# Performance work log

Hardware: AMD Instinct MI355X
Metric: run time of the kernel (lower is better)

Reference implementation:

```python
import jax, jax.numpy as jnp
import numpy as np

B, N, X, H = 128, 512, 128, 256  # batch, seq len, in features, hidden

_PARAM_SHAPES = [
    ("fg_w_c", (H,)), ("fg_w_h", (H, H)), ("fg_w_x", (H, X)), ("fg_b", (H,)),
    ("ig_w_c", (H,)), ("ig_w_h", (H, H)), ("ig_w_x", (H, X)), ("ig_b", (H,)),
    ("in_w_h", (H, H)), ("in_w_x", (H, X)), ("in_b", (H,)),
    ("og_w_cn", (H,)), ("og_w_h", (H, H)), ("og_w_x", (H, X)), ("og_b", (H,)), ("og_w_t", (H,)),
    ("tg1_w_x", (H, X)), ("tg1_w_t", (H,)), ("tg1_b", (H,)),
    ("tg2_w_x", (H, X)), ("tg2_w_t", (H,)), ("tg2_b", (H,)),
]


def setup_inputs() -> dict:
    key = jax.random.key(0)
    ks = jax.random.split(key, 2 + len(_PARAM_SHAPES))
    stdv = 1.0 / np.sqrt(H)  # torch __init__ re-inits all params uniform(-stdv, stdv)
    inp = {
        "x": jax.random.normal(ks[0], (B, N, X), jnp.float32),
        "t": jax.random.uniform(ks[1], (B, N, 1), jnp.float32),  # time intervals >= 0
    }
    for i, (name, shape) in enumerate(_PARAM_SHAPES):
        inp[name] = jax.random.uniform(ks[2 + i], shape, jnp.float32, -stdv, stdv)
    return inp


def reference(x, t,
              fg_w_c, fg_w_h, fg_w_x, fg_b,
              ig_w_c, ig_w_h, ig_w_x, ig_b,
              in_w_h, in_w_x, in_b,
              og_w_cn, og_w_h, og_w_x, og_b, og_w_t,
              tg1_w_x, tg1_w_t, tg1_b,
              tg2_w_x, tg2_w_t, tg2_b):
    # TimeLSTM_v3 with nn_type = NN_TYPE_LSTM_TIME2.
    # torch stores vector params as [H,1] and x_cur as [B,xm,1]; here squeezed to [H] / [B,xm].
    # Precompute all input-dependent (non-recurrent) gate terms over the whole sequence: [B,N,H]
    fg_x = jnp.einsum('bnx,hx->bnh', x, fg_w_x) + fg_b
    ig_x = jnp.einsum('bnx,hx->bnh', x, ig_w_x) + ig_b
    in_x = jnp.einsum('bnx,hx->bnh', x, in_w_x) + in_b
    og_x = jnp.einsum('bnx,hx->bnh', x, og_w_x) + og_w_t * t + og_b
    # Time gates depend only on x and t -> fully precomputable
    tm1 = jax.nn.sigmoid(jnp.einsum('bnx,hx->bnh', x, tg1_w_x) + jnp.tanh(tg1_w_t * t) + tg1_b)
    tm2 = jax.nn.sigmoid(jnp.einsum('bnx,hx->bnh', x, tg2_w_x) + jnp.tanh(tg2_w_t * t) + tg2_b)

    def step(carry, inputs):
        h, cm = carry  # each [B,H]
        fg_xt, ig_xt, in_xt, og_xt, tm1_t, tm2_t = inputs
        ig = jax.nn.sigmoid(ig_w_c * cm + h @ ig_w_h.T + ig_xt)
        fg = jax.nn.sigmoid(fg_w_c * cm + h @ fg_w_h.T + fg_xt)
        inn = jnp.tanh(h @ in_w_h.T + in_xt)
        cm_hat = fg * cm + ig * tm1_t * inn
        cm_new = fg * cm + ig * tm2_t * inn
        og = jax.nn.sigmoid(og_w_cn * cm_hat + h @ og_w_h.T + og_xt)
        h_new = og * jnp.tanh(cm_hat)
        return (h_new, cm_new), None

    seqs = tuple(jnp.moveaxis(a, 1, 0) for a in (fg_x, ig_x, in_x, og_x, tm1, tm2))  # [N,B,H]
    init = (jnp.zeros((x.shape[0], H), x.dtype), jnp.zeros((x.shape[0], H), x.dtype))
    (h, cm), _ = jax.lax.scan(step, init, seqs)
    return h, cm  # h: [B,H] (torch squeezes trailing 1), cm: [B,H]
```

## Files before the change

### kernel.cpp

```cpp
#include <hip/hip_runtime.h>
#include <math.h>

#define BATCH 128
#define SEQN  512
#define XF    128
#define HF    256
#define BC    16
#define HC    8
#define TCH   8
#define NBLK  256
#define NTHR  256
#define NGRP  8
#define GSZ   32

#define OFF_WX   0
#define OFF_G    6144
#define OFF_X    12288
#define OFF_CM   28672
#define OFF_TV   28800
#define OFF_COEF 28928
#define OFF_GO   29024
#define LDS_WORDS 29028
#define LDS_BYTES (LDS_WORDS * 4)

struct Params {
  const float* x;
  const float* t;
  const float* w_h[4];
  const float* w_x[6];
  const float* coef[12];
  float* h_buf;
  unsigned* flags;
  unsigned* round;
  float* out;
};

__device__ __forceinline__ float sigmoidf_(float v) { return 1.0f / (1.0f + __expf(-v)); }
__device__ __forceinline__ float tanhf_(float x) {
  const float e = __expf(2.0f * x);
  return 1.0f - 2.0f / (e + 1.0f);
}

__device__ __forceinline__ float swzx1(float v) { return __int_as_float(__builtin_amdgcn_ds_swizzle(__float_as_int(v), 0x041F)); }
__device__ __forceinline__ float swzx2(float v) { return __int_as_float(__builtin_amdgcn_ds_swizzle(__float_as_int(v), 0x081F)); }
__device__ __forceinline__ float swzx4(float v) { return __int_as_float(__builtin_amdgcn_ds_swizzle(__float_as_int(v), 0x101F)); }
__device__ __forceinline__ float swzx8(float v) { return __int_as_float(__builtin_amdgcn_ds_swizzle(__float_as_int(v), 0x201F)); }

__device__ __forceinline__ void post_arrive(unsigned* flags, int gi, int mi, unsigned val) {
  __syncthreads();
  if (threadIdx.x == 0) {
    __hip_atomic_store(&flags[(gi * GSZ + mi) * 16], val,
                       __ATOMIC_RELAXED, __HIP_MEMORY_SCOPE_AGENT);
  }
}

__device__ __forceinline__ void wave_wait(float* sm, const unsigned* flags,
                                          unsigned* round, int gi, int mi,
                                          unsigned target) {
  const int tid = threadIdx.x;
  if (mi == 0) {
    unsigned* go = (unsigned*)&sm[OFF_GO];
    if (tid < 64) {
      const bool need = tid < GSZ;
      const unsigned* f = &flags[(gi * GSZ + (tid & (GSZ - 1))) * 16];
      while (true) {
        unsigned v = need ? __hip_atomic_load(f, __ATOMIC_RELAXED, __HIP_MEMORY_SCOPE_AGENT)
                          : target;
        if (__all((int)(v >= target))) break;
      }
      if (tid == 0) {
        __hip_atomic_store(&round[gi * 16], target,
                           __ATOMIC_RELAXED, __HIP_MEMORY_SCOPE_AGENT);
        __hip_atomic_store(go, target, __ATOMIC_RELAXED, __HIP_MEMORY_SCOPE_WORKGROUP);
      }
    } else {
      while (__hip_atomic_load(go, __ATOMIC_RELAXED, __HIP_MEMORY_SCOPE_WORKGROUP) < target) {}
    }
  } else {
    const unsigned* r = &round[gi * 16];
    while (__hip_atomic_load(r, __ATOMIC_RELAXED, __HIP_MEMORY_SCOPE_AGENT) < target) {}
  }
  asm volatile("" ::: "memory");
}

__global__ __launch_bounds__(NTHR, 1) void timelstm_kernel(Params p) {
  extern __shared__ float sm[];
  const int tid = threadIdx.x;
  const int bid = blockIdx.x;
  const int gi = bid & 7;
  const int mi = bid >> 3;
  const int b0 = gi * BC;
  const int h0 = mi * HC;

  const int lane = tid & 63;
  const int bq = tid >> 6;
  const int kh = lane & 7;
  const int j  = lane >> 3;

  float wrs[4][32];
#pragma unroll
  for (int g = 0; g < 4; ++g)
#pragma unroll
    for (int q = 0; q < 8; ++q) {
      const float4 v = *(const float4*)&p.w_h[g][(size_t)(h0 + j) * HF + kh * 32 + q * 4];
      wrs[g][q * 4 + 0] = v.x; wrs[g][q * 4 + 1] = v.y;
      wrs[g][q * 4 + 2] = v.z; wrs[g][q * 4 + 3] = v.w;
    }
  for (int i = tid; i < 6 * 8 * 128; i += NTHR) {
    int g = i >> 10, jj = (i >> 7) & 7, k = i & 127;
    sm[OFF_WX + k * 48 + jj * 6 + g] = p.w_x[g][(h0 + jj) * XF + k];
  }
  if (tid < 96) sm[OFF_COEF + tid] = p.coef[tid >> 3][h0 + (tid & 7)];
  if (tid < 128) sm[OFF_CM + tid] = 0.0f;
  if (tid == 0) *(unsigned*)&sm[OFF_GO] = 0u;
  if (mi == 0) {
    unsigned long long* hbu = (unsigned long long*)p.h_buf + (size_t)b0 * (HF / 2);
    for (int i = tid; i < BC * HF / 2; i += NTHR) {
      __hip_atomic_store(&hbu[i], 0ull, __ATOMIC_RELAXED, __HIP_MEMORY_SCOPE_AGENT);
    }
  }
  post_arrive(p.flags, gi, mi, 1u);
  unsigned tstep = 1;
  int cur = 0;

  for (int tc0 = 0; tc0 < SEQN; tc0 += TCH) {
    __syncthreads();
    {
#pragma unroll
      for (int half = 0; half < 2; ++half) {
        float4 xr[8];
#pragma unroll
        for (int it = 0; it < 8; ++it) {
          const int ri = (half * 8 + it) * 8 + (tid >> 5);
          xr[it] = *(const float4*)&p.x[((size_t)(b0 + (ri >> 3)) * SEQN + (tc0 + (ri & 7))) * XF + (tid & 31) * 4];
        }
#pragma unroll
        for (int it = 0; it < 8; ++it) {
          const int ri = (half * 8 + it) * 8 + (tid >> 5);
          const int k0 = (tid & 31) * 4;
          const float xb[4] = {xr[it].x, xr[it].y, xr[it].z, xr[it].w};
#pragma unroll
          for (int u = 0; u < 4; ++u) {
            const int k = k0 + u;
            sm[OFF_X + k * 128 + (ri ^ (((k >> 2) & 7) << 2))] = xb[u];
          }
        }
      }
      if (tid < 128)
        sm[OFF_TV + tid] = p.t[(size_t)(b0 + (tid >> 3)) * SEQN + tc0 + (tid & 7)];
    }
    __syncthreads();
    {
      const int c = tid >> 3, r = tid & 7;
      const int c4 = c << 2;
      float a0[4], a1[4], a2[4], a3[4], a4[4], a5[4];
#pragma unroll
      for (int u = 0; u < 4; ++u) { a0[u]=0.f; a1[u]=0.f; a2[u]=0.f; a3[u]=0.f; a4[u]=0.f; a5[u]=0.f; }
      const float* wxp = &sm[OFF_WX + r * 6];
#pragma unroll 4
      for (int k = 0; k < XF; ++k) {
        const float4 xv = *(const float4*)&sm[OFF_X + k * 128 + (c4 ^ (((k >> 2) & 7) << 2))];
        const float2 wA = *(const float2*)&wxp[k * 48 + 0];
        const float2 wB = *(const float2*)&wxp[k * 48 + 2];
        const float2 wC = *(const float2*)&wxp[k * 48 + 4];
        const float xs[4] = {xv.x, xv.y, xv.z, xv.w};
#pragma unroll
        for (int u = 0; u < 4; ++u) {
          a0[u] += wA.x * xs[u]; a1[u] += wA.y * xs[u];
          a2[u] += wB.x * xs[u]; a3[u] += wB.y * xs[u];
          a4[u] += wC.x * xs[u]; a5[u] += wC.y * xs[u];
        }
      }
      const float cfg  = sm[OFF_COEF + 0 * 8 + r], cig  = sm[OFF_COEF + 1 * 8 + r];
      const float cin  = sm[OFF_COEF + 2 * 8 + r];
      const float cogb = sm[OFF_COEF + 3 * 8 + r], cogwt = sm[OFF_COEF + 4 * 8 + r];
      const float ct1w = sm[OFF_COEF + 5 * 8 + r], ct1b = sm[OFF_COEF + 6 * 8 + r];
      const float ct2w = sm[OFF_COEF + 7 * 8 + r], ct2b = sm[OFF_COEF + 8 * 8 + r];
#pragma unroll
      for (int u = 0; u < 4; ++u) {
        const int bt = c4 + u, b = bt >> 3, t = bt & 7;
        const float tv = sm[OFF_TV + bt];
        float* gp = &sm[OFF_G + t * 768 + b * 8 + r];
        gp[0]   = a0[u] + cfg;
        gp[128] = a1[u] + cig;
        gp[256] = a2[u] + cin;
        gp[384] = a3[u] + cogwt * tv + cogb;
        gp[512] = sigmoidf_(a4[u] + tanhf_(ct1w * tv) + ct1b);
        gp[640] = sigmoidf_(a5[u] + tanhf_(ct2w * tv) + ct2b);
      }
    }
    __syncthreads();

    for (int tt = 0; tt < TCH; ++tt) {
      wave_wait(sm, p.flags, p.round, gi, mi, tstep);
      {
        const unsigned long long* hsrc = (const unsigned long long*)
            (p.h_buf + (size_t)cur * BATCH * HF + (size_t)(b0 + (bq << 2)) * HF);
        unsigned long long v[4][2];
#pragma unroll
        for (int u = 0; u < 4; ++u) {
          const unsigned long long* src = hsrc + (size_t)u * (HF / 2) + lane * 2;
          v[u][0] = __hip_atomic_load(src,     __ATOMIC_RELAXED, __HIP_MEMORY_SCOPE_AGENT);
          v[u][1] = __hip_atomic_load(src + 1, __ATOMIC_RELAXED, __HIP_MEMORY_SCOPE_AGENT);
        }
        float f[4][4];
#pragma unroll
        for (int u = 0; u < 4; ++u) {
          union { unsigned long long u64; float2 f2; } x0, x1;
          x0.u64 = v[u][0]; x1.u64 = v[u][1];
          f[u][0] = x0.f2.x; f[u][1] = x0.f2.y; f[u][2] = x1.f2.x; f[u][3] = x1.f2.y;
        }
        const int swz = ((lane >> 3) & 7) << 2;
        const int wbase = OFF_X + (bq << 10);
#pragma unroll
        for (int e = 0; e < 4; ++e) {
          const int a = wbase + (((lane << 4) + (e << 2)) ^ swz);
          float2 lo = {f[0][e], f[1][e]};
          float2 hi = {f[2][e], f[3][e]};
          *(float2*)&sm[a]     = lo;
          *(float2*)&sm[a + 2] = hi;
        }
      }

      float acc[4][4];
#pragma unroll
      for (int bi = 0; bi < 4; ++bi)
#pragma unroll
        for (int g = 0; g < 4; ++g) acc[bi][g] = 0.f;

      const int hbase = OFF_X + (bq << 10) + (kh << 7);
      const int khx = kh << 2;
#pragma unroll
      for (int kk = 0; kk < 32; ++kk) {
        const int off = ((((kk & 7) << 2) ^ khx)) + ((kk >> 3) << 5);
        const float4 hv = *(const float4*)&sm[hbase + off];
        const float w0 = wrs[0][kk], w1 = wrs[1][kk], w2 = wrs[2][kk], w3 = wrs[3][kk];
        acc[0][0] += hv.x * w0; acc[0][1] += hv.x * w1; acc[0][2] += hv.x * w2; acc[0][3] += hv.x * w3;
        acc[1][0] += hv.y * w0; acc[1][1] += hv.y * w1; acc[1][2] += hv.y * w2; acc[1][3] += hv.y * w3;
        acc[2][0] += hv.z * w0; acc[2][1] += hv.z * w1; acc[2][2] += hv.z * w2; acc[2][3] += hv.z * w3;
        acc[3][0] += hv.w * w0; acc[3][1] += hv.w * w1; acc[3][2] += hv.w * w2; acc[3][3] += hv.w * w3;
      }

      const int kb0 = kh & 1, kb1 = (kh >> 1) & 1;
      float s1[2][4];
#pragma unroll
      for (int pp = 0; pp < 2; ++pp)
#pragma unroll
        for (int g = 0; g < 4; ++g) {
          const float mine  = kb0 ? acc[2 * pp + 1][g] : acc[2 * pp][g];
          const float yours = kb0 ? acc[2 * pp][g]     : acc[2 * pp + 1][g];
          s1[pp][g] = mine + swzx1(yours);
        }
      float s2[4];
#pragma unroll
      for (int g = 0; g < 4; ++g) {
        const float mine  = kb1 ? s1[1][g] : s1[0][g];
        const float yours = kb1 ? s1[0][g] : s1[1][g];
        s2[g] = mine + swzx2(yours);
      }
      float pre[4];
#pragma unroll
      for (int g = 0; g < 4; ++g) pre[g] = s2[g] + swzx4(s2[g]);

      {
        const int bi = kh & 3;
        const int b  = (bq << 2) + bi;
        const int ib = b * 8 + j;
        const float cm = sm[OFF_CM + ib];
        const float* gt = &sm[OFF_G + tt * 768 + ib];
        const float fgx = gt[0],   igx = gt[128], inx = gt[256];
        const float ogx = gt[384], tm1 = gt[512], tm2 = gt[640];
        const float igv = sigmoidf_(sm[OFF_COEF + 10 * 8 + j] * cm + pre[1] + igx);
        const float fgv = sigmoidf_(sm[OFF_COEF + 9 * 8 + j] * cm + pre[0] + fgx);
        const float inn = tanhf_(pre[2] + inx);
        const float cbase = fgv * cm, cinn = igv * inn;
        const float cmh = cbase + cinn * tm1;
        const float cmn = cbase + cinn * tm2;
        const float ogv = sigmoidf_(sm[OFF_COEF + 11 * 8 + j] * cmh + pre[3] + ogx);
        const float hn  = ogv * tanhf_(cmh);
        const float hn2 = swzx8(hn);
        if (kh < 4) {
          sm[OFF_CM + ib] = cmn;
          if (!(j & 1)) {
            union { float2 f; unsigned long long u; } cv;
            cv.f.x = hn; cv.f.y = hn2;
            unsigned long long* hdst =
                (unsigned long long*)(p.h_buf + (size_t)(cur ^ 1) * BATCH * HF +
                                      (size_t)(b0 + b) * HF + h0 + j);
            __hip_atomic_store(hdst, cv.u, __ATOMIC_RELAXED, __HIP_MEMORY_SCOPE_AGENT);
          }
          if (tc0 + tt == SEQN - 1) {
            p.out[(size_t)(b0 + b) * HF + h0 + j] = hn;
            p.out[(size_t)BATCH * HF + (size_t)(b0 + b) * HF + h0 + j] = cmn;
          }
        }
      }
      post_arrive(p.flags, gi, mi, tstep + 1);
      ++tstep;
      cur ^= 1;
    }
  }
}

extern "C" void kernel_launch(void* const* d_in, const int* in_sizes, int n_in,
                              void* d_out, int out_size, void* d_ws, size_t ws_size,
                              hipStream_t stream) {
  (void)in_sizes; (void)n_in; (void)out_size; (void)ws_size;
  Params p;
  p.x = (const float*)d_in[0];
  p.t = (const float*)d_in[1];
  p.w_h[0] = (const float*)d_in[3];
  p.w_h[1] = (const float*)d_in[7];
  p.w_h[2] = (const float*)d_in[10];
  p.w_h[3] = (const float*)d_in[14];
  p.w_x[0] = (const float*)d_in[4];
  p.w_x[1] = (const float*)d_in[8];
  p.w_x[2] = (const float*)d_in[11];
  p.w_x[3] = (const float*)d_in[15];
  p.w_x[4] = (const float*)d_in[18];
  p.w_x[5] = (const float*)d_in[21];
  p.coef[0]  = (const float*)d_in[5];
  p.coef[1]  = (const float*)d_in[9];
  p.coef[2]  = (const float*)d_in[12];
  p.coef[3]  = (const float*)d_in[16];
  p.coef[4]  = (const float*)d_in[17];
  p.coef[5]  = (const float*)d_in[19];
  p.coef[6]  = (const float*)d_in[20];
  p.coef[7]  = (const float*)d_in[22];
  p.coef[8]  = (const float*)d_in[23];
  p.coef[9]  = (const float*)d_in[2];
  p.coef[10] = (const float*)d_in[6];
  p.coef[11] = (const float*)d_in[13];
  p.flags = (unsigned*)d_ws;
  p.round = p.flags + NGRP * GSZ * 16;
  p.h_buf = (float*)((char*)d_ws + 32768);
  p.out = (float*)d_out;

  (void)hipMemsetAsync(d_ws, 0, 32768, stream);
  (void)hipFuncSetAttribute((const void*)timelstm_kernel,
                            hipFuncAttributeMaxDynamicSharedMemorySize, LDS_BYTES);
  timelstm_kernel<<<dim3(NBLK), dim3(NTHR), LDS_BYTES, stream>>>(p);
}
```

Baseline: 2.633 ms.

## Replace block-level step barrier with per-wave flag synchronization

Each wave now publishes its own progress flag and waits only on the matching wave (same batch quad) in the other blocks of its group, instead of a __syncthreads plus a single block flag per step. The master block uses one wave per batch quad to poll 32 flags and publishes a per-quad round counter, and the LDS go-word is removed. This is meant to cut the per-timestep cost of a full workgroup barrier and the serialized block-wide handoff on the recurrent critical path. It relies on each wave reading only the h rows its quad wrote, and on s_waitcnt vmcnt(0) with relaxed atomics giving enough ordering, which is a memory-ordering risk.

```diff
diff --git a/kernel.cpp b/kernel.cpp
--- a/kernel.cpp
+++ b/kernel.cpp
@@ -19,8 +19,7 @@
 #define OFF_CM   28672
 #define OFF_TV   28800
 #define OFF_COEF 28928
-#define OFF_GO   29024
-#define LDS_WORDS 29028
+#define LDS_WORDS 29024
 #define LDS_BYTES (LDS_WORDS * 4)
 
 struct Params {
@@ -46,38 +45,28 @@
 __device__ __forceinline__ float swzx4(float v) { return __int_as_float(__builtin_amdgcn_ds_swizzle(__float_as_int(v), 0x101F)); }
 __device__ __forceinline__ float swzx8(float v) { return __int_as_float(__builtin_amdgcn_ds_swizzle(__float_as_int(v), 0x201F)); }
 
-__device__ __forceinline__ void post_arrive(unsigned* flags, int gi, int mi, unsigned val) {
-  __syncthreads();
-  if (threadIdx.x == 0) {
-    __hip_atomic_store(&flags[(gi * GSZ + mi) * 16], val,
+__device__ __forceinline__ void post_wave(unsigned* flags, int gi, int mi, int bq, unsigned val) {
+  asm volatile("s_waitcnt vmcnt(0)" ::: "memory");
+  if ((threadIdx.x & 63) == 0) {
+    __hip_atomic_store(&flags[(gi * GSZ + mi) * 16 + bq], val,
                        __ATOMIC_RELAXED, __HIP_MEMORY_SCOPE_AGENT);
   }
 }
 
-__device__ __forceinline__ void wave_wait(float* sm, const unsigned* flags,
-                                          unsigned* round, int gi, int mi,
+__device__ __forceinline__ void wave_wait(const unsigned* flags, unsigned* round,
+                                          int gi, int mi, int bq, int lane,
                                           unsigned target) {
-  const int tid = threadIdx.x;
   if (mi == 0) {
-    unsigned* go = (unsigned*)&sm[OFF_GO];
-    if (tid < 64) {
-      const bool need = tid < GSZ;
-      const unsigned* f = &flags[(gi * GSZ + (tid & (GSZ - 1))) * 16];
-      while (true) {
-        unsigned v = need ? __hip_atomic_load(f, __ATOMIC_RELAXED, __HIP_MEMORY_SCOPE_AGENT)
-                          : target;
-        if (__all((int)(v >= target))) break;
-      }
-      if (tid == 0) {
-        __hip_atomic_store(&round[gi * 16], target,
-                           __ATOMIC_RELAXED, __HIP_MEMORY_SCOPE_AGENT);
-        __hip_atomic_store(go, target, __ATOMIC_RELAXED, __HIP_MEMORY_SCOPE_WORKGROUP);
-      }
-    } else {
-      while (__hip_atomic_load(go, __ATOMIC_RELAXED, __HIP_MEMORY_SCOPE_WORKGROUP) < target) {}
-    }
+    const unsigned* f = &flags[(gi * GSZ + (lane & 31)) * 16 + bq];
+    while (true) {
+      const unsigned v = __hip_atomic_load(f, __ATOMIC_RELAXED, __HIP_MEMORY_SCOPE_AGENT);
+      if (__all((int)(v >= target))) break;
+    }
+    if (lane == 0)
+      __hip_atomic_store(&round[(gi * 4 + bq) * 16], target,
+                         __ATOMIC_RELAXED, __HIP_MEMORY_SCOPE_AGENT);
   } else {
-    const unsigned* r = &round[gi * 16];
+    const unsigned* r = &round[(gi * 4 + bq) * 16];
     while (__hip_atomic_load(r, __ATOMIC_RELAXED, __HIP_MEMORY_SCOPE_AGENT) < target) {}
   }
   asm volatile("" ::: "memory");
@@ -112,14 +101,17 @@
   }
   if (tid < 96) sm[OFF_COEF + tid] = p.coef[tid >> 3][h0 + (tid & 7)];
   if (tid < 128) sm[OFF_CM + tid] = 0.0f;
-  if (tid == 0) *(unsigned*)&sm[OFF_GO] = 0u;
   if (mi == 0) {
-    unsigned long long* hbu = (unsigned long long*)p.h_buf + (size_t)b0 * (HF / 2);
-    for (int i = tid; i < BC * HF / 2; i += NTHR) {
-      __hip_atomic_store(&hbu[i], 0ull, __ATOMIC_RELAXED, __HIP_MEMORY_SCOPE_AGENT);
-    }
-  }
-  post_arrive(p.flags, gi, mi, 1u);
+    unsigned long long* zb = (unsigned long long*)p.h_buf +
+                             (size_t)(b0 + (bq << 2)) * (HF / 2);
+#pragma unroll
+    for (int q = 0; q < 8; ++q) {
+      __hip_atomic_store(&zb[q * 64 + lane], 0ull,
+                         __ATOMIC_RELAXED, __HIP_MEMORY_SCOPE_AGENT);
+    }
+  }
+  post_wave(p.flags, gi, mi, bq, 1u);
+  __syncthreads();
   unsigned tstep = 1;
   int cur = 0;
 
@@ -192,7 +184,7 @@
     __syncthreads();
 
     for (int tt = 0; tt < TCH; ++tt) {
-      wave_wait(sm, p.flags, p.round, gi, mi, tstep);
+      wave_wait(p.flags, p.round, gi, mi, bq, lane, tstep);
       {
         const unsigned long long* hsrc = (const unsigned long long*)
             (p.h_buf + (size_t)cur * BATCH * HF + (size_t)(b0 + (bq << 2)) * HF);
@@ -295,7 +287,7 @@
           }
         }
       }
-      post_arrive(p.flags, gi, mi, tstep + 1);
+      post_wave(p.flags, gi, mi, bq, tstep + 1);
       ++tstep;
       cur ^= 1;
     }
```

Result: slower. 3.140 ms (+19.2%).

## Prefetch next chunk's x and t into registers during the recurrent steps

Applied to the files above, without the earlier changes.

Global loads of x and t for the next time chunk are issued into registers before the recurrent steps of the current chunk, so their latency overlaps the serial recurrence. The non-recurrent gate projection (phase A) then runs right after the chunk's steps, from registers instead of freshly loaded data. The h staging buffer gets its own LDS region so it no longer aliases the x staging area. The block-wide barriers around phase A are dropped because each wave now writes and reads only its own x rows. This relies on wave-local LDS ordering and adds about 64 more registers per thread.

```diff
diff --git a/kernel.cpp b/kernel.cpp
--- a/kernel.cpp
+++ b/kernel.cpp
@@ -15,12 +15,12 @@
 
 #define OFF_WX   0
 #define OFF_G    6144
-#define OFF_X    12288
-#define OFF_CM   28672
-#define OFF_TV   28800
-#define OFF_COEF 28928
-#define OFF_GO   29024
-#define LDS_WORDS 29028
+#define OFF_XS   12288
+#define OFF_H    28672
+#define OFF_CM   32768
+#define OFF_COEF 32896
+#define OFF_GO   32992
+#define LDS_WORDS 32996
 #define LDS_BYTES (LDS_WORDS * 4)
 
 struct Params {
@@ -96,6 +96,8 @@
   const int bq = tid >> 6;
   const int kh = lane & 7;
   const int j  = lane >> 3;
+  const int rr = tid & 7;
+  const int c4 = (tid >> 3) << 2;
 
   float wrs[4][32];
 #pragma unroll
@@ -120,77 +122,79 @@
     }
   }
   post_arrive(p.flags, gi, mi, 1u);
+
+  float4 xr[16];
+  float  tvn[4];
+  auto prefetch = [&](int tc) {
+#pragma unroll
+    for (int q = 0; q < 16; ++q) {
+      const int bt = (bq << 5) + q * 2 + (lane >> 5);
+      xr[q] = *(const float4*)&p.x[((size_t)(b0 + (bt >> 3)) * SEQN + (tc + (bt & 7))) * XF + (lane & 31) * 4];
+    }
+#pragma unroll
+    for (int u = 0; u < 4; ++u) {
+      const int bt = c4 + u;
+      tvn[u] = p.t[(size_t)(b0 + (bt >> 3)) * SEQN + tc + (bt & 7)];
+    }
+  };
+
+  auto phaseA = [&]() {
+#pragma unroll
+    for (int q = 0; q < 16; ++q) {
+      const int bt = (bq << 5) + q * 2 + (lane >> 5);
+      const int k0 = (lane & 31) * 4;
+      const float xb[4] = {xr[q].x, xr[q].y, xr[q].z, xr[q].w};
+#pragma unroll
+      for (int u = 0; u < 4; ++u) {
+        const int k = k0 + u;
+        sm[OFF_XS + k * 128 + (bt ^ (((k >> 2) & 7) << 2))] = xb[u];
+      }
+    }
+    float a0[4], a1[4], a2[4], a3[4], a4[4], a5[4];
+#pragma unroll
+    for (int u = 0; u < 4; ++u) { a0[u]=0.f; a1[u]=0.f; a2[u]=0.f; a3[u]=0.f; a4[u]=0.f; a5[u]=0.f; }
+    const float* wxp = &sm[OFF_WX + rr * 6];
+#pragma unroll 4
+    for (int k = 0; k < XF; ++k) {
+      const float4 xv = *(const float4*)&sm[OFF_XS + k * 128 + (c4 ^ (((k >> 2) & 7) << 2))];
+      const float2 wA = *(const float2*)&wxp[k * 48 + 0];
+      const float2 wB = *(const float2*)&wxp[k * 48 + 2];
+      const float2 wC = *(const float2*)&wxp[k * 48 + 4];
+      const float xs[4] = {xv.x, xv.y, xv.z, xv.w};
+#pragma unroll
+      for (int u = 0; u < 4; ++u) {
+        a0[u] += wA.x * xs[u]; a1[u] += wA.y * xs[u];
+        a2[u] += wB.x * xs[u]; a3[u] += wB.y * xs[u];
+        a4[u] += wC.x * xs[u]; a5[u] += wC.y * xs[u];
+      }
+    }
+    const float cfg  = sm[OFF_COEF + 0 * 8 + rr], cig  = sm[OFF_COEF + 1 * 8 + rr];
+    const float cin  = sm[OFF_COEF + 2 * 8 + rr];
+    const float cogb = sm[OFF_COEF + 3 * 8 + rr], cogwt = sm[OFF_COEF + 4 * 8 + rr];
+    const float ct1w = sm[OFF_COEF + 5 * 8 + rr], ct1b = sm[OFF_COEF + 6 * 8 + rr];
+    const float ct2w = sm[OFF_COEF + 7 * 8 + rr], ct2b = sm[OFF_COEF + 8 * 8 + rr];
+#pragma unroll
+    for (int u = 0; u < 4; ++u) {
+      const int bt = c4 + u, b = bt >> 3, t = bt & 7;
+      const float tv = tvn[u];
+      float* gp = &sm[OFF_G + t * 768 + b * 8 + rr];
+      gp[0]   = a0[u] + cfg;
+      gp[128] = a1[u] + cig;
+      gp[256] = a2[u] + cin;
+      gp[384] = a3[u] + cogwt * tv + cogb;
+      gp[512] = sigmoidf_(a4[u] + tanhf_(ct1w * tv) + ct1b);
+      gp[640] = sigmoidf_(a5[u] + tanhf_(ct2w * tv) + ct2b);
+    }
+  };
+
+  prefetch(0);
+  phaseA();
+  prefetch(TCH);
+
   unsigned tstep = 1;
   int cur = 0;
 
   for (int tc0 = 0; tc0 < SEQN; tc0 += TCH) {
-    __syncthreads();
-    {
-#pragma unroll
-      for (int half = 0; half < 2; ++half) {
-        float4 xr[8];
-#pragma unroll
-        for (int it = 0; it < 8; ++it) {
-          const int ri = (half * 8 + it) * 8 + (tid >> 5);
-          xr[it] = *(const float4*)&p.x[((size_t)(b0 + (ri >> 3)) * SEQN + (tc0 + (ri & 7))) * XF + (tid & 31) * 4];
-        }
-#pragma unroll
-        for (int it = 0; it < 8; ++it) {
-          const int ri = (half * 8 + it) * 8 + (tid >> 5);
-          const int k0 = (tid & 31) * 4;
-          const float xb[4] = {xr[it].x, xr[it].y, xr[it].z, xr[it].w};
-#pragma unroll
-          for (int u = 0; u < 4; ++u) {
-            const int k = k0 + u;
-            sm[OFF_X + k * 128 + (ri ^ (((k >> 2) & 7) << 2))] = xb[u];
-          }
-        }
-      }
-      if (tid < 128)
-        sm[OFF_TV + tid] = p.t[(size_t)(b0 + (tid >> 3)) * SEQN + tc0 + (tid & 7)];
-    }
-    __syncthreads();
-    {
-      const int c = tid >> 3, r = tid & 7;
-      const int c4 = c << 2;
-      float a0[4], a1[4], a2[4], a3[4], a4[4], a5[4];
-#pragma unroll
-      for (int u = 0; u < 4; ++u) { a0[u]=0.f; a1[u]=0.f; a2[u]=0.f; a3[u]=0.f; a4[u]=0.f; a5[u]=0.f; }
-      const float* wxp = &sm[OFF_WX + r * 6];
-#pragma unroll 4
-      for (int k = 0; k < XF; ++k) {
-        const float4 xv = *(const float4*)&sm[OFF_X + k * 128 + (c4 ^ (((k >> 2) & 7) << 2))];
-        const float2 wA = *(const float2*)&wxp[k * 48 + 0];
-        const float2 wB = *(const float2*)&wxp[k * 48 + 2];
-        const float2 wC = *(const float2*)&wxp[k * 48 + 4];
-        const float xs[4] = {xv.x, xv.y, xv.z, xv.w};
-#pragma unroll
-        for (int u = 0; u < 4; ++u) {
-          a0[u] += wA.x * xs[u]; a1[u] += wA.y * xs[u];
-          a2[u] += wB.x * xs[u]; a3[u] += wB.y * xs[u];
-          a4[u] += wC.x * xs[u]; a5[u] += wC.y * xs[u];
-        }
-      }
-      const float cfg  = sm[OFF_COEF + 0 * 8 + r], cig  = sm[OFF_COEF + 1 * 8 + r];
-      const float cin  = sm[OFF_COEF + 2 * 8 + r];
-      const float cogb = sm[OFF_COEF + 3 * 8 + r], cogwt = sm[OFF_COEF + 4 * 8 + r];
-      const float ct1w = sm[OFF_COEF + 5 * 8 + r], ct1b = sm[OFF_COEF + 6 * 8 + r];
-      const float ct2w = sm[OFF_COEF + 7 * 8 + r], ct2b = sm[OFF_COEF + 8 * 8 + r];
-#pragma unroll
-      for (int u = 0; u < 4; ++u) {
-        const int bt = c4 + u, b = bt >> 3, t = bt & 7;
-        const float tv = sm[OFF_TV + bt];
-        float* gp = &sm[OFF_G + t * 768 + b * 8 + r];
-        gp[0]   = a0[u] + cfg;
-        gp[128] = a1[u] + cig;
-        gp[256] = a2[u] + cin;
-        gp[384] = a3[u] + cogwt * tv + cogb;
-        gp[512] = sigmoidf_(a4[u] + tanhf_(ct1w * tv) + ct1b);
-        gp[640] = sigmoidf_(a5[u] + tanhf_(ct2w * tv) + ct2b);
-      }
-    }
-    __syncthreads();
-
     for (int tt = 0; tt < TCH; ++tt) {
       wave_wait(sm, p.flags, p.round, gi, mi, tstep);
       {
@@ -211,7 +215,7 @@
           f[u][0] = x0.f2.x; f[u][1] = x0.f2.y; f[u][2] = x1.f2.x; f[u][3] = x1.f2.y;
         }
         const int swz = ((lane >> 3) & 7) << 2;
-        const int wbase = OFF_X + (bq << 10);
+        const int wbase = OFF_H + (bq << 10);
 #pragma unroll
         for (int e = 0; e < 4; ++e) {
           const int a = wbase + (((lane << 4) + (e << 2)) ^ swz);
@@ -228,7 +232,7 @@
 #pragma unroll
         for (int g = 0; g < 4; ++g) acc[bi][g] = 0.f;
 
-      const int hbase = OFF_X + (bq << 10) + (kh << 7);
+      const int hbase = OFF_H + (bq << 10) + (kh << 7);
       const int khx = kh << 2;
 #pragma unroll
       for (int kk = 0; kk < 32; ++kk) {
@@ -298,6 +302,11 @@
       post_arrive(p.flags, gi, mi, tstep + 1);
       ++tstep;
       cur ^= 1;
+    }
+
+    if (tc0 + TCH < SEQN) {
+      phaseA();
+      if (tc0 + 2 * TCH < SEQN) prefetch(tc0 + 2 * TCH);
     }
   }
 }
```

Result: slower. 3.203 ms (+21.6%).

## Repartition recurrent work into 32 groups of 4 batches by 32 hidden units

Applied to the files above, without the earlier changes.

Changes the block decomposition from 8 batch groups of 16 rows with 8 hidden units per block to 32 batch groups of 4 rows with 32 hidden units per block. Each synchronisation group shrinks from 32 to 8 blocks, which cuts the per-step barrier fan-in and the amount of h each block must read from global memory every step. The cost is that each block now keeps 4x more input-projection weights in LDS, and the LDS layouts, swizzles and index mappings are all rewritten to match.

```diff
diff --git a/kernel.cpp b/kernel.cpp
--- a/kernel.cpp
+++ b/kernel.cpp
@@ -5,22 +5,22 @@
 #define SEQN  512
 #define XF    128
 #define HF    256
-#define BC    16
-#define HC    8
+#define BC    4
+#define HC    32
 #define TCH   8
 #define NBLK  256
 #define NTHR  256
-#define NGRP  8
-#define GSZ   32
+#define NGRP  32
+#define GSZ   8
 
 #define OFF_WX   0
-#define OFF_G    6144
-#define OFF_X    12288
-#define OFF_CM   28672
-#define OFF_TV   28800
-#define OFF_COEF 28928
-#define OFF_GO   29024
-#define LDS_WORDS 29028
+#define OFF_G    24576
+#define OFF_X    30720
+#define OFF_CM   34816
+#define OFF_TV   34944
+#define OFF_COEF 34976
+#define OFF_GO   35360
+#define LDS_WORDS 35364
 #define LDS_BYTES (LDS_WORDS * 4)
 
 struct Params {
@@ -87,30 +87,33 @@
   extern __shared__ float sm[];
   const int tid = threadIdx.x;
   const int bid = blockIdx.x;
-  const int gi = bid & 7;
-  const int mi = bid >> 3;
+  const int gi = bid & 31;
+  const int mi = bid >> 5;
   const int b0 = gi * BC;
   const int h0 = mi * HC;
 
   const int lane = tid & 63;
-  const int bq = tid >> 6;
+  const int wav = tid >> 6;
   const int kh = lane & 7;
-  const int j  = lane >> 3;
+  const int jm = wav * 8 + (lane >> 3);
+  const int jp = tid & 31;
+  const int c4 = (tid >> 5) << 2;
 
   float wrs[4][32];
 #pragma unroll
   for (int g = 0; g < 4; ++g)
 #pragma unroll
     for (int q = 0; q < 8; ++q) {
-      const float4 v = *(const float4*)&p.w_h[g][(size_t)(h0 + j) * HF + kh * 32 + q * 4];
+      const float4 v = *(const float4*)&p.w_h[g][(size_t)(h0 + jm) * HF + kh * 32 + q * 4];
       wrs[g][q * 4 + 0] = v.x; wrs[g][q * 4 + 1] = v.y;
       wrs[g][q * 4 + 2] = v.z; wrs[g][q * 4 + 3] = v.w;
     }
-  for (int i = tid; i < 6 * 8 * 128; i += NTHR) {
-    int g = i >> 10, jj = (i >> 7) & 7, k = i & 127;
-    sm[OFF_WX + k * 48 + jj * 6 + g] = p.w_x[g][(h0 + jj) * XF + k];
-  }
-  if (tid < 96) sm[OFF_COEF + tid] = p.coef[tid >> 3][h0 + (tid & 7)];
+  for (int i = tid; i < 6 * 32 * 128; i += NTHR) {
+    const int g = i >> 12, rem = i & 4095, jj = rem >> 7, k = rem & 127;
+    sm[OFF_WX + k * 192 + jj * 6 + g] = p.w_x[g][(size_t)(h0 + jj) * XF + k];
+  }
+  for (int i = tid; i < 12 * 32; i += NTHR)
+    sm[OFF_COEF + i] = p.coef[i >> 5][h0 + (i & 31)];
   if (tid < 128) sm[OFF_CM + tid] = 0.0f;
   if (tid == 0) *(unsigned*)&sm[OFF_GO] = 0u;
   if (mi == 0) {
@@ -127,42 +130,32 @@
     __syncthreads();
     {
 #pragma unroll
-      for (int half = 0; half < 2; ++half) {
-        float4 xr[8];
-#pragma unroll
-        for (int it = 0; it < 8; ++it) {
-          const int ri = (half * 8 + it) * 8 + (tid >> 5);
-          xr[it] = *(const float4*)&p.x[((size_t)(b0 + (ri >> 3)) * SEQN + (tc0 + (ri & 7))) * XF + (tid & 31) * 4];
-        }
-#pragma unroll
-        for (int it = 0; it < 8; ++it) {
-          const int ri = (half * 8 + it) * 8 + (tid >> 5);
-          const int k0 = (tid & 31) * 4;
-          const float xb[4] = {xr[it].x, xr[it].y, xr[it].z, xr[it].w};
-#pragma unroll
-          for (int u = 0; u < 4; ++u) {
-            const int k = k0 + u;
-            sm[OFF_X + k * 128 + (ri ^ (((k >> 2) & 7) << 2))] = xb[u];
-          }
-        }
-      }
-      if (tid < 128)
+      for (int it = 0; it < 4; ++it) {
+        const int bt = it * 8 + (tid >> 5);
+        const int k0 = (tid & 31) * 4;
+        const float4 v = *(const float4*)&p.x[((size_t)(b0 + (bt >> 3)) * SEQN + (tc0 + (bt & 7))) * XF + k0];
+        const float xb[4] = {v.x, v.y, v.z, v.w};
+#pragma unroll
+        for (int u = 0; u < 4; ++u) {
+          const int k = k0 + u;
+          sm[OFF_X + k * 32 + (bt ^ (((k >> 2) & 7) << 2))] = xb[u];
+        }
+      }
+      if (tid < 32)
         sm[OFF_TV + tid] = p.t[(size_t)(b0 + (tid >> 3)) * SEQN + tc0 + (tid & 7)];
     }
     __syncthreads();
     {
-      const int c = tid >> 3, r = tid & 7;
-      const int c4 = c << 2;
       float a0[4], a1[4], a2[4], a3[4], a4[4], a5[4];
 #pragma unroll
       for (int u = 0; u < 4; ++u) { a0[u]=0.f; a1[u]=0.f; a2[u]=0.f; a3[u]=0.f; a4[u]=0.f; a5[u]=0.f; }
-      const float* wxp = &sm[OFF_WX + r * 6];
+      const float* wxp = &sm[OFF_WX + jp * 6];
 #pragma unroll 4
       for (int k = 0; k < XF; ++k) {
-        const float4 xv = *(const float4*)&sm[OFF_X + k * 128 + (c4 ^ (((k >> 2) & 7) << 2))];
-        const float2 wA = *(const float2*)&wxp[k * 48 + 0];
-        const float2 wB = *(const float2*)&wxp[k * 48 + 2];
-        const float2 wC = *(const float2*)&wxp[k * 48 + 4];
+        const float4 xv = *(const float4*)&sm[OFF_X + k * 32 + (c4 ^ (((k >> 2) & 7) << 2))];
+        const float2 wA = *(const float2*)&wxp[k * 192 + 0];
+        const float2 wB = *(const float2*)&wxp[k * 192 + 2];
+        const float2 wC = *(const float2*)&wxp[k * 192 + 4];
         const float xs[4] = {xv.x, xv.y, xv.z, xv.w};
 #pragma unroll
         for (int u = 0; u < 4; ++u) {
@@ -171,16 +164,16 @@
           a4[u] += wC.x * xs[u]; a5[u] += wC.y * xs[u];
         }
       }
-      const float cfg  = sm[OFF_COEF + 0 * 8 + r], cig  = sm[OFF_COEF + 1 * 8 + r];
-      const float cin  = sm[OFF_COEF + 2 * 8 + r];
-      const float cogb = sm[OFF_COEF + 3 * 8 + r], cogwt = sm[OFF_COEF + 4 * 8 + r];
-      const float ct1w = sm[OFF_COEF + 5 * 8 + r], ct1b = sm[OFF_COEF + 6 * 8 + r];
-      const float ct2w = sm[OFF_COEF + 7 * 8 + r], ct2b = sm[OFF_COEF + 8 * 8 + r];
+      const float cfg  = sm[OFF_COEF + 0 * 32 + jp], cig  = sm[OFF_COEF + 1 * 32 + jp];
+      const float cin  = sm[OFF_COEF + 2 * 32 + jp];
+      const float cogb = sm[OFF_COEF + 3 * 32 + jp], cogwt = sm[OFF_COEF + 4 * 32 + jp];
+      const float ct1w = sm[OFF_COEF + 5 * 32 + jp], ct1b = sm[OFF_COEF + 6 * 32 + jp];
+      const float ct2w = sm[OFF_COEF + 7 * 32 + jp], ct2b = sm[OFF_COEF + 8 * 32 + jp];
 #pragma unroll
       for (int u = 0; u < 4; ++u) {
         const int bt = c4 + u, b = bt >> 3, t = bt & 7;
         const float tv = sm[OFF_TV + bt];
-        float* gp = &sm[OFF_G + t * 768 + b * 8 + r];
+        float* gp = &sm[OFF_G + t * 768 + jp * 4 + b];
         gp[0]   = a0[u] + cfg;
         gp[128] = a1[u] + cig;
         gp[256] = a2[u] + cin;
@@ -195,30 +188,28 @@
       wave_wait(sm, p.flags, p.round, gi, mi, tstep);
       {
         const unsigned long long* hsrc = (const unsigned long long*)
-            (p.h_buf + (size_t)cur * BATCH * HF + (size_t)(b0 + (bq << 2)) * HF);
+            (p.h_buf + (size_t)cur * BATCH * HF) + (size_t)b0 * (HF / 2);
         unsigned long long v[4][2];
 #pragma unroll
-        for (int u = 0; u < 4; ++u) {
-          const unsigned long long* src = hsrc + (size_t)u * (HF / 2) + lane * 2;
-          v[u][0] = __hip_atomic_load(src,     __ATOMIC_RELAXED, __HIP_MEMORY_SCOPE_AGENT);
-          v[u][1] = __hip_atomic_load(src + 1, __ATOMIC_RELAXED, __HIP_MEMORY_SCOPE_AGENT);
-        }
-        float f[4][4];
-#pragma unroll
-        for (int u = 0; u < 4; ++u) {
-          union { unsigned long long u64; float2 f2; } x0, x1;
-          x0.u64 = v[u][0]; x1.u64 = v[u][1];
-          f[u][0] = x0.f2.x; f[u][1] = x0.f2.y; f[u][2] = x1.f2.x; f[u][3] = x1.f2.y;
-        }
-        const int swz = ((lane >> 3) & 7) << 2;
-        const int wbase = OFF_X + (bq << 10);
-#pragma unroll
-        for (int e = 0; e < 4; ++e) {
-          const int a = wbase + (((lane << 4) + (e << 2)) ^ swz);
-          float2 lo = {f[0][e], f[1][e]};
-          float2 hi = {f[2][e], f[3][e]};
-          *(float2*)&sm[a]     = lo;
-          *(float2*)&sm[a + 2] = hi;
+        for (int r = 0; r < 4; ++r) {
+          v[r][0] = __hip_atomic_load(&hsrc[r * 128 + lane],      __ATOMIC_RELAXED, __HIP_MEMORY_SCOPE_AGENT);
+          v[r][1] = __hip_atomic_load(&hsrc[r * 128 + lane + 64], __ATOMIC_RELAXED, __HIP_MEMORY_SCOPE_AGENT);
+        }
+        const int wbase = OFF_X + (wav << 10);
+#pragma unroll
+        for (int pp = 0; pp < 2; ++pp) {
+          float2 f0, f1, f2, f3;
+          { union { unsigned long long u; float2 f; } c; c.u = v[0][pp]; f0 = c.f; }
+          { union { unsigned long long u; float2 f; } c; c.u = v[1][pp]; f1 = c.f; }
+          { union { unsigned long long u; float2 f; } c; c.u = v[2][pp]; f2 = c.f; }
+          { union { unsigned long long u; float2 f; } c; c.u = v[3][pp]; f3 = c.f; }
+          const int k0 = 2 * lane + pp * 128;
+          const int a0w = wbase + ((k0 << 2) ^ ((((k0) >> 5) & 7) << 2));
+          const int a1w = wbase + (((k0 + 1) << 2) ^ ((((k0 + 1) >> 5) & 7) << 2));
+          float4 lo = {f0.x, f1.x, f2.x, f3.x};
+          float4 hi = {f0.y, f1.y, f2.y, f3.y};
+          *(float4*)&sm[a0w] = lo;
+          *(float4*)&sm[a1w] = hi;
         }
       }
 
@@ -228,11 +219,11 @@
 #pragma unroll
         for (int g = 0; g < 4; ++g) acc[bi][g] = 0.f;
 
-      const int hbase = OFF_X + (bq << 10) + (kh << 7);
+      const int hbase = OFF_X + (wav << 10) + kh * 128;
       const int khx = kh << 2;
 #pragma unroll
       for (int kk = 0; kk < 32; ++kk) {
-        const int off = ((((kk & 7) << 2) ^ khx)) + ((kk >> 3) << 5);
+        const int off = ((kk >> 3) << 5) + ((((kk ^ kh) & 7)) << 2);
         const float4 hv = *(const float4*)&sm[hbase + off];
         const float w0 = wrs[0][kk], w1 = wrs[1][kk], w2 = wrs[2][kk], w3 = wrs[3][kk];
         acc[0][0] += hv.x * w0; acc[0][1] += hv.x * w1; acc[0][2] += hv.x * w2; acc[0][3] += hv.x * w3;
@@ -263,35 +254,34 @@
       for (int g = 0; g < 4; ++g) pre[g] = s2[g] + swzx4(s2[g]);
 
       {
-        const int bi = kh & 3;
-        const int b  = (bq << 2) + bi;
-        const int ib = b * 8 + j;
+        const int b  = kh & 3;
+        const int ib = jm * 4 + b;
         const float cm = sm[OFF_CM + ib];
         const float* gt = &sm[OFF_G + tt * 768 + ib];
         const float fgx = gt[0],   igx = gt[128], inx = gt[256];
         const float ogx = gt[384], tm1 = gt[512], tm2 = gt[640];
-        const float igv = sigmoidf_(sm[OFF_COEF + 10 * 8 + j] * cm + pre[1] + igx);
-        const float fgv = sigmoidf_(sm[OFF_COEF + 9 * 8 + j] * cm + pre[0] + fgx);
+        const float igv = sigmoidf_(sm[OFF_COEF + 10 * 32 + jm] * cm + pre[1] + igx);
+        const float fgv = sigmoidf_(sm[OFF_COEF + 9 * 32 + jm] * cm + pre[0] + fgx);
         const float inn = tanhf_(pre[2] + inx);
         const float cbase = fgv * cm, cinn = igv * inn;
         const float cmh = cbase + cinn * tm1;
         const float cmn = cbase + cinn * tm2;
-        const float ogv = sigmoidf_(sm[OFF_COEF + 11 * 8 + j] * cmh + pre[3] + ogx);
+        const float ogv = sigmoidf_(sm[OFF_COEF + 11 * 32 + jm] * cmh + pre[3] + ogx);
         const float hn  = ogv * tanhf_(cmh);
         const float hn2 = swzx8(hn);
         if (kh < 4) {
           sm[OFF_CM + ib] = cmn;
-          if (!(j & 1)) {
+          if (!(jm & 1)) {
             union { float2 f; unsigned long long u; } cv;
             cv.f.x = hn; cv.f.y = hn2;
             unsigned long long* hdst =
                 (unsigned long long*)(p.h_buf + (size_t)(cur ^ 1) * BATCH * HF +
-                                      (size_t)(b0 + b) * HF + h0 + j);
+                                      (size_t)(b0 + b) * HF + h0 + jm);
             __hip_atomic_store(hdst, cv.u, __ATOMIC_RELAXED, __HIP_MEMORY_SCOPE_AGENT);
           }
           if (tc0 + tt == SEQN - 1) {
-            p.out[(size_t)(b0 + b) * HF + h0 + j] = hn;
-            p.out[(size_t)BATCH * HF + (size_t)(b0 + b) * HF + h0 + j] = cmn;
+            p.out[(size_t)(b0 + b) * HF + h0 + jm] = hn;
+            p.out[(size_t)BATCH * HF + (size_t)(b0 + b) * HF + h0 + jm] = cmn;
           }
         }
       }
```

After: 2.630 ms (median of 2 runs). About the same (-0.1%).
